# Optimization experiments

Measured on AMD Instinct MI355X. Metric: run time of the kernel, lower is better.

Reference implementation:

```python
import jax, jax.numpy as jnp
import numpy as np

N_NODES = 100000
N_EDGES = 1600000
D_IN = 64
D_OUT = 64
CLAMP = -10000.0  # scatter_'max' post-clamp threshold from the source


def setup_inputs() -> dict:
    key = jax.random.key(0)
    k1, k2, k3, k4, k5 = jax.random.split(key, 5)
    n_feat = jax.random.normal(k1, (N_NODES, D_IN), dtype=jnp.float32)
    src = jax.random.randint(k2, (N_EDGES,), 0, N_NODES, dtype=jnp.int64)
    dst = jax.random.randint(k3, (N_EDGES,), 0, N_NODES, dtype=jnp.int64)
    W = jax.random.normal(k4, (2 * D_IN, D_OUT), dtype=jnp.float32) / np.sqrt(2 * D_IN)
    b = jax.random.normal(k5, (D_OUT,), dtype=jnp.float32) * 0.01
    return {"n_feat": n_feat, "src": src, "dst": dst, "W": W, "b": b}


def reference(n_feat, src, dst, W, b):
    # gather endpoint features and form relative messages: [E, d]
    diff = n_feat[src] - n_feat[dst]
    # scatter-max aggregate onto destination nodes: [N, d]
    agg = jax.ops.segment_max(diff, dst, num_segments=n_feat.shape[0])
    # torch_scatter fills empty slots with lowest value; source clamps out<-10000 to 0
    agg = jnp.where(agg < CLAMP, 0.0, agg)
    # concat original + aggregated, then MLP = Linear + ReLU: [N, 2d] @ [2d, out]
    h = jnp.concatenate([n_feat, agg], axis=1)
    return jax.nn.relu(h @ W + b)
```

## Files before the change

kernel.cpp:

```cpp
#include <hip/hip_runtime.h>
#include <hip/hip_bf16.h>

#define D 64
#define CLAMP_V -10000.0f
#define SBSHIFT 9
#define SBN 512
#define MAXSB 256
#define HCHUNK 4096
#define SCHUNK 4096
#define SORT_THREADS 1024

typedef __bf16 bf16x4 __attribute__((ext_vector_type(4)));
typedef __bf16 bf16x8 __attribute__((ext_vector_type(8)));
typedef float floatx4 __attribute__((ext_vector_type(4)));
typedef unsigned short u16x2 __attribute__((ext_vector_type(2)));
typedef short s16x2 __attribute__((ext_vector_type(2)));

__device__ __forceinline__ unsigned pkmax(unsigned a, unsigned b) {
    u16x2 r = __builtin_elementwise_max(__builtin_bit_cast(u16x2, a),
                                        __builtin_bit_cast(u16x2, b));
    return __builtin_bit_cast(unsigned, r);
}
__device__ __forceinline__ uint4 pkmax4(uint4 a, uint4 b) {
    uint4 r;
    r.x = pkmax(a.x, b.x); r.y = pkmax(a.y, b.y);
    r.z = pkmax(a.z, b.z); r.w = pkmax(a.w, b.w);
    return r;
}
__device__ __forceinline__ unsigned pk_ord_encode(unsigned g) {
    s16x2 t = __builtin_bit_cast(s16x2, g) >> 15;
    unsigned m = __builtin_bit_cast(unsigned, t) & 0x7FFF7FFFu;
    return g ^ (m | 0x80008000u);
}
__device__ __forceinline__ unsigned pk_ord_decode(unsigned e) {
    s16x2 t = __builtin_bit_cast(s16x2, e) >> 15;
    unsigned m = (~__builtin_bit_cast(unsigned, t)) & 0x7FFF7FFFu;
    return e ^ (m | 0x80008000u);
}
__device__ __forceinline__ unsigned seg_finish2(unsigned encm, unsigned encs) {
    unsigned raw = pk_ord_decode(encm);
    unsigned xr  = pk_ord_decode(encs);
    float v0 = __uint_as_float(raw << 16);
    float v1 = __uint_as_float(raw & 0xFFFF0000u);
    float x0 = __uint_as_float(xr << 16);
    float x1 = __uint_as_float(xr & 0xFFFF0000u);
    float r0 = v0 - x0; r0 = (r0 >= CLAMP_V) ? r0 : 0.0f;
    float r1 = v1 - x1; r1 = (r1 >= CLAMP_V) ? r1 : 0.0f;
    __bf16 b0 = (__bf16)r0, b1 = (__bf16)r1;
    return ((unsigned)__builtin_bit_cast(unsigned short, b1) << 16)
         |  (unsigned)__builtin_bit_cast(unsigned short, b0);
}

__global__ __launch_bounds__(256) void prep_kernel(
        const float* __restrict__ nf, unsigned* __restrict__ nfenc, int n4,
        const int* __restrict__ dst, unsigned* __restrict__ ghist,
        int nE, int nbSB,
        const float* __restrict__ W, __bf16* __restrict__ wfrag,
        int histBlocks, int wBlock) {
    __shared__ unsigned h[MAXSB];
    int blk = blockIdx.x, t = threadIdx.x;
    int i = blk * 256 + t;
    if (i < n4) {
        float4 v = ((const float4*)nf)[i];
        __bf16 b0 = (__bf16)v.x, b1 = (__bf16)v.y;
        __bf16 b2 = (__bf16)v.z, b3 = (__bf16)v.w;
        unsigned d0 = ((unsigned)__builtin_bit_cast(unsigned short, b1) << 16)
                    |  (unsigned)__builtin_bit_cast(unsigned short, b0);
        unsigned d1 = ((unsigned)__builtin_bit_cast(unsigned short, b3) << 16)
                    |  (unsigned)__builtin_bit_cast(unsigned short, b2);
        uint2 e; e.x = pk_ord_encode(d0); e.y = pk_ord_encode(d1);
        ((uint2*)nfenc)[i] = e;
    }
    if (blk < histBlocks) {
        if (t < MAXSB) h[t] = 0;
        __syncthreads();
        int e0 = blk * HCHUNK;
        int ec = nE - e0; if (ec > HCHUNK) ec = HCHUNK;
        for (int k = t; k < ec; k += 256) atomicAdd(&h[dst[e0 + k] >> SBSHIFT], 1u);
        __syncthreads();
        if (t < (unsigned)nbSB && h[t]) atomicAdd(&ghist[t], h[t]);
    }
    if (blk == wBlock) {
        for (int idx = t; idx < 2 * D * D; idx += 256) {
            int k = idx >> 6, n = idx & 63;
            int ks = k >> 5, r = k & 31, quad = r >> 3, j = r & 7;
            int c = n >> 4, l16 = n & 15;
            int fidx = (((ks * 4 + c) * 64) + quad * 16 + l16) * 8 + j;
            wfrag[fidx] = (__bf16)W[idx];
        }
    }
}

__global__ __launch_bounds__(256) void scan_sb(
        const unsigned* __restrict__ ghist, unsigned* __restrict__ base,
        unsigned* __restrict__ cursor, int nbSB) {
    __shared__ unsigned ts[256];
    int t = threadIdx.x;
    unsigned v = (t < nbSB) ? ghist[t] : 0u;
    ts[t] = v; __syncthreads();
    for (int off = 1; off < 256; off <<= 1) {
        unsigned x = (t >= off) ? ts[t - off] : 0u;
        __syncthreads();
        ts[t] += x;
        __syncthreads();
    }
    if (t < nbSB) {
        unsigned ex = ts[t] - v;
        base[t] = ex; cursor[t] = ex;
        if (t == nbSB - 1) base[nbSB] = ts[t];
    }
}

__global__ __launch_bounds__(256) void sb_scatter(
        const int* __restrict__ src, const int* __restrict__ dst,
        unsigned* __restrict__ cursor, unsigned* __restrict__ packed,
        int nE, int nbSB) {
    __shared__ unsigned cop[MAXSB];
    __shared__ unsigned short lb16[MAXSB];
    __shared__ unsigned gbase[MAXSB];
    __shared__ unsigned payload[SCHUNK];
    __shared__ unsigned char sbid[SCHUNK];
    __shared__ unsigned ts[256];
    int t = threadIdx.x;
    int e0 = blockIdx.x * SCHUNK;
    int ec = nE - e0; if (ec > SCHUNK) ec = SCHUNK;

    if (t < MAXSB) cop[t] = 0;
    __syncthreads();
    for (int i = t; i < ec; i += 256)
        atomicAdd(&cop[dst[e0 + i] >> SBSHIFT], 1u);
    __syncthreads();
    unsigned c = (t < nbSB) ? (cop[t] & 0xFFFFu) : 0u;
    ts[t] = c; __syncthreads();
    for (int o = 1; o < 256; o <<= 1) {
        unsigned x = (t >= o) ? ts[t - o] : 0u;
        __syncthreads();
        ts[t] += x;
        __syncthreads();
    }
    if (t < nbSB) {
        lb16[t] = (unsigned short)(ts[t] - c);
        if (c) gbase[t] = atomicAdd(&cursor[t], c);
    }
    __syncthreads();
    for (int i = t; i < ec; i += 256) {
        int e = e0 + i;
        int d = dst[e];
        int b = d >> SBSHIFT;
        unsigned p = atomicAdd(&cop[b], 0x10000u) >> 16;
        unsigned pos = (unsigned)lb16[b] + p;
        payload[pos] = ((unsigned)(d & (SBN - 1)) << 17) | (unsigned)src[e];
        sbid[pos] = (unsigned char)b;
    }
    __syncthreads();
    for (int i = t; i < ec; i += 256) {
        unsigned b = sbid[i];
        packed[gbase[b] + ((unsigned)i - (unsigned)lb16[b])] = payload[i];
    }
}

__global__ __launch_bounds__(SORT_THREADS) void sb_sort(
        const unsigned* __restrict__ packed1, const unsigned* __restrict__ base,
        unsigned* __restrict__ packed2, unsigned* __restrict__ nodestart,
        int nN) {
    __shared__ unsigned cnt[SBN];
    __shared__ unsigned ts[SBN];
    int sb = blockIdx.x, t = threadIdx.x;
    unsigned beg = base[sb], end = base[sb + 1];
    if (t < SBN) cnt[t] = 0;
    __syncthreads();
    for (unsigned i = beg + t; i < end; i += SORT_THREADS)
        atomicAdd(&cnt[packed1[i] >> 17], 1u);
    __syncthreads();
    unsigned s = (t < SBN) ? cnt[t] : 0u;
    if (t < SBN) ts[t] = s;
    __syncthreads();
    for (int o = 1; o < SBN; o <<= 1) {
        unsigned x = 0;
        if (t < SBN && t >= o) x = ts[t - o];
        __syncthreads();
        if (t < SBN) ts[t] += x;
        __syncthreads();
    }
    if (t < SBN) {
        unsigned ex = ts[t] - s;
        cnt[t] = ex;
        int n0 = sb * SBN;
        if (n0 + t <= nN) nodestart[n0 + t] = beg + ex;
    }
    __syncthreads();
    for (unsigned i = beg + t; i < end; i += SORT_THREADS) {
        unsigned e = packed1[i];
        unsigned p = atomicAdd(&cnt[e >> 17], 1u);
        packed2[beg + p] = e & 0x1FFFFu;
    }
}

__global__ __launch_bounds__(256) void seg_direct(
        const uint4* __restrict__ enc4,
        const unsigned* __restrict__ packed2,
        const unsigned* __restrict__ nodestart,
        uint4* __restrict__ agg4,
        int nN) {
    int t = threadIdx.x;
    int ln = t & 63;
    int grp = ln >> 3;
    int col = ln & 7;
    int n = blockIdx.x * 32 + (t >> 6) * 8 + grp;
    if (n >= nN) return;
    unsigned rb = nodestart[n], re = nodestart[n + 1];
    unsigned deg = re - rb;
    const uint4* ec = enc4 + col;
    uint4 a0 = {0,0,0,0}, a1 = {0,0,0,0}, a2 = {0,0,0,0}, a3 = {0,0,0,0};
    unsigned i = 0;
    for (; i + 8 <= deg; i += 8) {
        unsigned e0 = packed2[rb + i];
        unsigned e1 = packed2[rb + i + 1];
        unsigned e2 = packed2[rb + i + 2];
        unsigned e3 = packed2[rb + i + 3];
        unsigned e4 = packed2[rb + i + 4];
        unsigned e5 = packed2[rb + i + 5];
        unsigned e6 = packed2[rb + i + 6];
        unsigned e7 = packed2[rb + i + 7];
        uint4 g0 = ec[(size_t)e0 * 8];
        uint4 g1 = ec[(size_t)e1 * 8];
        uint4 g2 = ec[(size_t)e2 * 8];
        uint4 g3 = ec[(size_t)e3 * 8];
        uint4 g4 = ec[(size_t)e4 * 8];
        uint4 g5 = ec[(size_t)e5 * 8];
        uint4 g6 = ec[(size_t)e6 * 8];
        uint4 g7 = ec[(size_t)e7 * 8];
        a0 = pkmax4(a0, g0);
        a1 = pkmax4(a1, g1);
        a2 = pkmax4(a2, g2);
        a3 = pkmax4(a3, g3);
        a0 = pkmax4(a0, g4);
        a1 = pkmax4(a1, g5);
        a2 = pkmax4(a2, g6);
        a3 = pkmax4(a3, g7);
    }
    for (; i + 4 <= deg; i += 4) {
        unsigned e0 = packed2[rb + i];
        unsigned e1 = packed2[rb + i + 1];
        unsigned e2 = packed2[rb + i + 2];
        unsigned e3 = packed2[rb + i + 3];
        uint4 g0 = ec[(size_t)e0 * 8];
        uint4 g1 = ec[(size_t)e1 * 8];
        uint4 g2 = ec[(size_t)e2 * 8];
        uint4 g3 = ec[(size_t)e3 * 8];
        a0 = pkmax4(a0, g0);
        a1 = pkmax4(a1, g1);
        a2 = pkmax4(a2, g2);
        a3 = pkmax4(a3, g3);
    }
    for (; i < deg; ++i) {
        unsigned e0 = packed2[rb + i];
        a0 = pkmax4(a0, ec[(size_t)e0 * 8]);
    }
    uint4 m = pkmax4(pkmax4(a0, a1), pkmax4(a2, a3));
    uint4 es = ec[(size_t)n * 8];
    uint4 o;
    o.x = seg_finish2(m.x, es.x);
    o.y = seg_finish2(m.y, es.y);
    o.z = seg_finish2(m.z, es.z);
    o.w = seg_finish2(m.w, es.w);
    agg4[(size_t)n * 8 + col] = o;
}

__global__ __launch_bounds__(256) void node_mlp_mfma(
        const unsigned* __restrict__ nfencu,
        const __bf16* __restrict__ agg16,
        float* __restrict__ out,
        const __bf16* __restrict__ wfrag,
        const float* __restrict__ bias,
        int nTiles, int nN) {
    int lane = threadIdx.x & 63;
    int quad = lane >> 4;
    int l16  = lane & 15;
    int waveGlobal = blockIdx.x * 4 + (threadIdx.x >> 6);
    int nWaves = gridDim.x * 4;

    bf16x8 bfrag[4][4];
    #pragma unroll
    for (int c = 0; c < 4; ++c)
        #pragma unroll
        for (int ks = 0; ks < 4; ++ks)
            bfrag[c][ks] = *(const bf16x8*)(wfrag + ((size_t)((ks * 4 + c) * 64 + lane)) * 8);
    float bv[4];
    #pragma unroll
    for (int c = 0; c < 4; ++c) bv[c] = bias[c * 16 + l16];

    for (int t = waveGlobal; t < nTiles; t += nWaves) {
        int n0 = t * 16;
        int rowA = n0 + l16;
        if (rowA >= nN) rowA = nN - 1;
        const unsigned* nfr = nfencu + (size_t)rowA * 32;
        const __bf16*   agr = agg16  + (size_t)rowA * D;

        floatx4 acc[4] = {{0,0,0,0},{0,0,0,0},{0,0,0,0},{0,0,0,0}};
        #pragma unroll
        for (int ks = 0; ks < 4; ++ks) {
            bf16x8 a;
            if (ks < 2) {
                uint4 w = *(const uint4*)(nfr + ks * 16 + quad * 4);
                w.x = pk_ord_decode(w.x); w.y = pk_ord_decode(w.y);
                w.z = pk_ord_decode(w.z); w.w = pk_ord_decode(w.w);
                a = __builtin_bit_cast(bf16x8, w);
            } else {
                a = *(const bf16x8*)(agr + (ks - 2) * 32 + quad * 8);
            }
            #pragma unroll
            for (int c = 0; c < 4; ++c)
                acc[c] = __builtin_amdgcn_mfma_f32_16x16x32_bf16(
                             a, bfrag[c][ks], acc[c], 0, 0, 0);
        }
        #pragma unroll
        for (int r = 0; r < 4; ++r) {
            int row = n0 + quad * 4 + r;
            if (row < nN) {
                #pragma unroll
                for (int c = 0; c < 4; ++c) {
                    float vv = acc[c][r] + bv[c];
                    out[(size_t)row * D + c * 16 + l16] = fmaxf(vv, 0.0f);
                }
            }
        }
    }
}

extern "C" void kernel_launch(void* const* d_in, const int* in_sizes, int n_in,
                              void* d_out, int out_size, void* d_ws, size_t ws_size,
                              hipStream_t stream) {
    const float* nf  = (const float*)d_in[0];
    const int*   src = (const int*)d_in[1];
    const int*   dst = (const int*)d_in[2];
    const float* W   = (const float*)d_in[3];
    const float* b   = (const float*)d_in[4];
    float* out = (float*)d_out;

    int nN = in_sizes[0] / D;
    int nE = in_sizes[1];
    int nbSB = (nN + SBN - 1) / SBN;

    char* wsb = (char*)d_ws;
    size_t nfB  = (((size_t)nN * D * 2) + 255) & ~(size_t)255;
    size_t pkB  = (((size_t)nE * 4)     + 255) & ~(size_t)255;
    unsigned* nfenc  = (unsigned*)wsb;
    __bf16*   agg16  = (__bf16*)(wsb + nfB);
    unsigned* packed1 = (unsigned*)(wsb + 2 * nfB);
    unsigned* ghist  = (unsigned*)(wsb + 2 * nfB + pkB);
    unsigned* base   = (unsigned*)(wsb + 2 * nfB + pkB + 4 * MAXSB);
    unsigned* cursor = (unsigned*)(wsb + 2 * nfB + pkB + 4 * MAXSB + 4 * (MAXSB + 2));
    __bf16*   wfrag  = (__bf16*)(wsb + 2 * nfB + pkB + 4 * MAXSB + 8 * (MAXSB + 2));
    unsigned* nodestart = (unsigned*)(wsb + 2 * nfB + pkB + 4 * MAXSB
                                      + 8 * (MAXSB + 2) + 32768);
    unsigned* packed2 = (unsigned*)d_out;

    hipMemsetAsync(ghist, 0, (size_t)nbSB * 4, stream);

    int n4 = nN * D / 4;
    int convBlocks = (n4 + 255) / 256;
    int histBlocks = (nE + HCHUNK - 1) / HCHUNK;
    int gridPrep = convBlocks > histBlocks ? convBlocks : histBlocks;
    prep_kernel<<<gridPrep, 256, 0, stream>>>(nf, nfenc, n4, dst, ghist,
                                              nE, nbSB, W, wfrag,
                                              histBlocks, gridPrep - 1);

    scan_sb<<<1, 256, 0, stream>>>(ghist, base, cursor, nbSB);

    int nbS = (nE + SCHUNK - 1) / SCHUNK;
    sb_scatter<<<nbS, 256, 0, stream>>>(src, dst, cursor, packed1, nE, nbSB);

    sb_sort<<<nbSB, SORT_THREADS, 0, stream>>>(packed1, base, packed2,
                                               nodestart, nN);

    int segBlocks = (nN + 31) / 32;
    seg_direct<<<segBlocks, 256, 0, stream>>>(
        (const uint4*)nfenc, packed2, nodestart, (uint4*)agg16, nN);

    int nTiles = (nN + 15) / 16;
    node_mlp_mfma<<<768, 256, 0, stream>>>(nfenc, agg16, out, wfrag, b,
                                           nTiles, nN);
}
```

Measured before the change: 179.7 us.

## Fuse segment-max aggregation with MFMA node MLP via shared-memory tile

Merges the segment-max gather kernel and the MFMA MLP kernel into one launch. Each block aggregates 32 nodes into a shared-memory bf16 tile, then four waves each compute half the output columns of a 16-row tile. This removes the global write and re-read of the aggregated features and one kernel launch. packed2 moves from the output buffer into workspace, since the output is now written during the same kernel. In exchange, every block reloads its weight fragments and the MLP phase uses fewer MFMAs per wave.

```diff
diff --git a/kernel.cpp b/kernel.cpp
--- a/kernel.cpp
+++ b/kernel.cpp
@@ -196,108 +196,102 @@
     }
 }
 
-__global__ __launch_bounds__(256) void seg_direct(
+__global__ __launch_bounds__(256) void seg_mlp(
         const uint4* __restrict__ enc4,
         const unsigned* __restrict__ packed2,
         const unsigned* __restrict__ nodestart,
-        uint4* __restrict__ agg4,
+        const __bf16* __restrict__ wfrag,
+        const float* __restrict__ bias,
+        float* __restrict__ out,
         int nN) {
+    __shared__ __bf16 aggs[32][72];
     int t = threadIdx.x;
-    int ln = t & 63;
+    int wv = t >> 6, ln = t & 63;
     int grp = ln >> 3;
     int col = ln & 7;
-    int n = blockIdx.x * 32 + (t >> 6) * 8 + grp;
-    if (n >= nN) return;
-    unsigned rb = nodestart[n], re = nodestart[n + 1];
-    unsigned deg = re - rb;
-    const uint4* ec = enc4 + col;
-    uint4 a0 = {0,0,0,0}, a1 = {0,0,0,0}, a2 = {0,0,0,0}, a3 = {0,0,0,0};
-    unsigned i = 0;
-    for (; i + 8 <= deg; i += 8) {
-        unsigned e0 = packed2[rb + i];
-        unsigned e1 = packed2[rb + i + 1];
-        unsigned e2 = packed2[rb + i + 2];
-        unsigned e3 = packed2[rb + i + 3];
-        unsigned e4 = packed2[rb + i + 4];
-        unsigned e5 = packed2[rb + i + 5];
-        unsigned e6 = packed2[rb + i + 6];
-        unsigned e7 = packed2[rb + i + 7];
-        uint4 g0 = ec[(size_t)e0 * 8];
-        uint4 g1 = ec[(size_t)e1 * 8];
-        uint4 g2 = ec[(size_t)e2 * 8];
-        uint4 g3 = ec[(size_t)e3 * 8];
-        uint4 g4 = ec[(size_t)e4 * 8];
-        uint4 g5 = ec[(size_t)e5 * 8];
-        uint4 g6 = ec[(size_t)e6 * 8];
-        uint4 g7 = ec[(size_t)e7 * 8];
-        a0 = pkmax4(a0, g0);
-        a1 = pkmax4(a1, g1);
-        a2 = pkmax4(a2, g2);
-        a3 = pkmax4(a3, g3);
-        a0 = pkmax4(a0, g4);
-        a1 = pkmax4(a1, g5);
-        a2 = pkmax4(a2, g6);
-        a3 = pkmax4(a3, g7);
-    }
-    for (; i + 4 <= deg; i += 4) {
-        unsigned e0 = packed2[rb + i];
-        unsigned e1 = packed2[rb + i + 1];
-        unsigned e2 = packed2[rb + i + 2];
-        unsigned e3 = packed2[rb + i + 3];
-        uint4 g0 = ec[(size_t)e0 * 8];
-        uint4 g1 = ec[(size_t)e1 * 8];
-        uint4 g2 = ec[(size_t)e2 * 8];
-        uint4 g3 = ec[(size_t)e3 * 8];
-        a0 = pkmax4(a0, g0);
-        a1 = pkmax4(a1, g1);
-        a2 = pkmax4(a2, g2);
-        a3 = pkmax4(a3, g3);
-    }
-    for (; i < deg; ++i) {
-        unsigned e0 = packed2[rb + i];
-        a0 = pkmax4(a0, ec[(size_t)e0 * 8]);
-    }
-    uint4 m = pkmax4(pkmax4(a0, a1), pkmax4(a2, a3));
-    uint4 es = ec[(size_t)n * 8];
-    uint4 o;
-    o.x = seg_finish2(m.x, es.x);
-    o.y = seg_finish2(m.y, es.y);
-    o.z = seg_finish2(m.z, es.z);
-    o.w = seg_finish2(m.w, es.w);
-    agg4[(size_t)n * 8 + col] = o;
-}
-
-__global__ __launch_bounds__(256) void node_mlp_mfma(
-        const unsigned* __restrict__ nfencu,
-        const __bf16* __restrict__ agg16,
-        float* __restrict__ out,
-        const __bf16* __restrict__ wfrag,
-        const float* __restrict__ bias,
-        int nTiles, int nN) {
-    int lane = threadIdx.x & 63;
-    int quad = lane >> 4;
-    int l16  = lane & 15;
-    int waveGlobal = blockIdx.x * 4 + (threadIdx.x >> 6);
-    int nWaves = gridDim.x * 4;
-
-    bf16x8 bfrag[4][4];
-    #pragma unroll
-    for (int c = 0; c < 4; ++c)
+    int n0 = blockIdx.x * 32;
+    int n = n0 + wv * 8 + grp;
+    if (n < nN) {
+        unsigned rb = nodestart[n], re = nodestart[n + 1];
+        unsigned deg = re - rb;
+        const uint4* ec = enc4 + col;
+        uint4 a0 = {0,0,0,0}, a1 = {0,0,0,0}, a2 = {0,0,0,0}, a3 = {0,0,0,0};
+        unsigned i = 0;
+        for (; i + 8 <= deg; i += 8) {
+            unsigned e0 = packed2[rb + i];
+            unsigned e1 = packed2[rb + i + 1];
+            unsigned e2 = packed2[rb + i + 2];
+            unsigned e3 = packed2[rb + i + 3];
+            unsigned e4 = packed2[rb + i + 4];
+            unsigned e5 = packed2[rb + i + 5];
+            unsigned e6 = packed2[rb + i + 6];
+            unsigned e7 = packed2[rb + i + 7];
+            uint4 g0 = ec[(size_t)e0 * 8];
+            uint4 g1 = ec[(size_t)e1 * 8];
+            uint4 g2 = ec[(size_t)e2 * 8];
+            uint4 g3 = ec[(size_t)e3 * 8];
+            uint4 g4 = ec[(size_t)e4 * 8];
+            uint4 g5 = ec[(size_t)e5 * 8];
+            uint4 g6 = ec[(size_t)e6 * 8];
+            uint4 g7 = ec[(size_t)e7 * 8];
+            a0 = pkmax4(a0, g0);
+            a1 = pkmax4(a1, g1);
+            a2 = pkmax4(a2, g2);
+            a3 = pkmax4(a3, g3);
+            a0 = pkmax4(a0, g4);
+            a1 = pkmax4(a1, g5);
+            a2 = pkmax4(a2, g6);
+            a3 = pkmax4(a3, g7);
+        }
+        for (; i + 4 <= deg; i += 4) {
+            unsigned e0 = packed2[rb + i];
+            unsigned e1 = packed2[rb + i + 1];
+            unsigned e2 = packed2[rb + i + 2];
+            unsigned e3 = packed2[rb + i + 3];
+            uint4 g0 = ec[(size_t)e0 * 8];
+            uint4 g1 = ec[(size_t)e1 * 8];
+            uint4 g2 = ec[(size_t)e2 * 8];
+            uint4 g3 = ec[(size_t)e3 * 8];
+            a0 = pkmax4(a0, g0);
+            a1 = pkmax4(a1, g1);
+            a2 = pkmax4(a2, g2);
+            a3 = pkmax4(a3, g3);
+        }
+        for (; i < deg; ++i) {
+            unsigned e0 = packed2[rb + i];
+            a0 = pkmax4(a0, ec[(size_t)e0 * 8]);
+        }
+        uint4 m = pkmax4(pkmax4(a0, a1), pkmax4(a2, a3));
+        uint4 es = ec[(size_t)n * 8];
+        uint4 o;
+        o.x = seg_finish2(m.x, es.x);
+        o.y = seg_finish2(m.y, es.y);
+        o.z = seg_finish2(m.z, es.z);
+        o.w = seg_finish2(m.w, es.w);
+        *(uint4*)&aggs[wv * 8 + grp][col * 8] = o;
+    }
+    __syncthreads();
+    int l16 = ln & 15, quad = ln >> 4;
+    int tile = wv >> 1, cpair = wv & 1;
+    int tn0 = n0 + tile * 16;
+    if (tn0 < nN) {
+        bf16x8 bfrag[2][4];
         #pragma unroll
-        for (int ks = 0; ks < 4; ++ks)
-            bfrag[c][ks] = *(const bf16x8*)(wfrag + ((size_t)((ks * 4 + c) * 64 + lane)) * 8);
-    float bv[4];
-    #pragma unroll
-    for (int c = 0; c < 4; ++c) bv[c] = bias[c * 16 + l16];
-
-    for (int t = waveGlobal; t < nTiles; t += nWaves) {
-        int n0 = t * 16;
-        int rowA = n0 + l16;
+        for (int cc = 0; cc < 2; ++cc) {
+            int c = cpair * 2 + cc;
+            #pragma unroll
+            for (int ks = 0; ks < 4; ++ks)
+                bfrag[cc][ks] = *(const bf16x8*)(
+                    wfrag + ((size_t)((ks * 4 + c) * 64 + ln)) * 8);
+        }
+        float bv[2];
+        #pragma unroll
+        for (int cc = 0; cc < 2; ++cc)
+            bv[cc] = bias[(cpair * 2 + cc) * 16 + l16];
+        int rowA = tn0 + l16;
         if (rowA >= nN) rowA = nN - 1;
-        const unsigned* nfr = nfencu + (size_t)rowA * 32;
-        const __bf16*   agr = agg16  + (size_t)rowA * D;
-
-        floatx4 acc[4] = {{0,0,0,0},{0,0,0,0},{0,0,0,0},{0,0,0,0}};
+        const unsigned* nfr = (const unsigned*)enc4 + (size_t)rowA * 32;
+        floatx4 acc[2] = {{0,0,0,0},{0,0,0,0}};
         #pragma unroll
         for (int ks = 0; ks < 4; ++ks) {
             bf16x8 a;
@@ -307,21 +301,23 @@
                 w.z = pk_ord_decode(w.z); w.w = pk_ord_decode(w.w);
                 a = __builtin_bit_cast(bf16x8, w);
             } else {
-                a = *(const bf16x8*)(agr + (ks - 2) * 32 + quad * 8);
+                a = *(const bf16x8*)&aggs[tile * 16 + l16]
+                                         [(ks - 2) * 32 + quad * 8];
             }
             #pragma unroll
-            for (int c = 0; c < 4; ++c)
-                acc[c] = __builtin_amdgcn_mfma_f32_16x16x32_bf16(
-                             a, bfrag[c][ks], acc[c], 0, 0, 0);
+            for (int cc = 0; cc < 2; ++cc)
+                acc[cc] = __builtin_amdgcn_mfma_f32_16x16x32_bf16(
+                              a, bfrag[cc][ks], acc[cc], 0, 0, 0);
         }
         #pragma unroll
         for (int r = 0; r < 4; ++r) {
-            int row = n0 + quad * 4 + r;
+            int row = tn0 + quad * 4 + r;
             if (row < nN) {
                 #pragma unroll
-                for (int c = 0; c < 4; ++c) {
-                    float vv = acc[c][r] + bv[c];
-                    out[(size_t)row * D + c * 16 + l16] = fmaxf(vv, 0.0f);
+                for (int cc = 0; cc < 2; ++cc) {
+                    float vv = acc[cc][r] + bv[cc];
+                    out[(size_t)row * D + (cpair * 2 + cc) * 16 + l16] =
+                        fmaxf(vv, 0.0f);
                 }
             }
         }
@@ -346,7 +342,7 @@
     size_t nfB  = (((size_t)nN * D * 2) + 255) & ~(size_t)255;
     size_t pkB  = (((size_t)nE * 4)     + 255) & ~(size_t)255;
     unsigned* nfenc  = (unsigned*)wsb;
-    __bf16*   agg16  = (__bf16*)(wsb + nfB);
+    unsigned* packed2 = (unsigned*)(wsb + nfB);
     unsigned* packed1 = (unsigned*)(wsb + 2 * nfB);
     unsigned* ghist  = (unsigned*)(wsb + 2 * nfB + pkB);
     unsigned* base   = (unsigned*)(wsb + 2 * nfB + pkB + 4 * MAXSB);
@@ -354,7 +350,6 @@
     __bf16*   wfrag  = (__bf16*)(wsb + 2 * nfB + pkB + 4 * MAXSB + 8 * (MAXSB + 2));
     unsigned* nodestart = (unsigned*)(wsb + 2 * nfB + pkB + 4 * MAXSB
                                       + 8 * (MAXSB + 2) + 32768);
-    unsigned* packed2 = (unsigned*)d_out;
 
     hipMemsetAsync(ghist, 0, (size_t)nbSB * 4, stream);
 
@@ -375,10 +370,6 @@
                                                nodestart, nN);
 
     int segBlocks = (nN + 31) / 32;
-    seg_direct<<<segBlocks, 256, 0, stream>>>(
-        (const uint4*)nfenc, packed2, nodestart, (uint4*)agg16, nN);
-
-    int nTiles = (nN + 15) / 16;
-    node_mlp_mfma<<<768, 256, 0, stream>>>(nfenc, agg16, out, wfrag, b,
-                                           nTiles, nN);
-}
+    seg_mlp<<<segBlocks, 256, 0, stream>>>(
+        (const uint4*)nfenc, packed2, nodestart, wfrag, b, out, nN);
+}
```

Result: no change. 181.3 us (+0.9%).
